# Performance work log

Hardware: AMD Instinct MI355X
Metric: run time of the kernel (lower is better)

## Reference

```python
import jax, jax.numpy as jnp
import numpy as np

D_MODEL, D_FF, N_EXPERTS, P = 512, 2048, 16, 128
B, S = 8, 512


def setup_inputs() -> dict:
    key = jax.random.key(0)
    ks = jax.random.split(key, 16)
    T = B * S
    g = lambda k, shape, fan: (jax.random.normal(k, shape, jnp.float32) * (fan ** -0.5))
    return {
        "x": jax.random.normal(ks[0], (B, S, D_MODEL), jnp.float32),
        "h_prev": jax.random.normal(ks[1], (T, P), jnp.float32),
        # projector: Linear(d_model -> p)
        "Wp": g(ks[2], (P, D_MODEL), D_MODEL), "bp": jnp.zeros((P,), jnp.float32),
        # GRUCell(p, p): torch layout [3p, p] in (r, z, n) order
        "W_ih": g(ks[3], (3 * P, P), P), "W_hh": g(ks[4], (3 * P, P), P),
        "b_ih": jnp.zeros((3 * P,), jnp.float32), "b_hh": jnp.zeros((3 * P,), jnp.float32),
        # router: Linear(p -> num_experts)
        "Wr": g(ks[5], (N_EXPERTS, P), P), "br": jnp.zeros((N_EXPERTS,), jnp.float32),
        # experts: Linear(d, dff) -> ReLU -> Linear(dff, d), stacked over experts
        "W1": g(ks[6], (N_EXPERTS, D_MODEL, D_FF), D_MODEL),
        "b1": jnp.zeros((N_EXPERTS, D_FF), jnp.float32),
        "W2": g(ks[7], (N_EXPERTS, D_FF, D_MODEL), D_FF),
        "b2": jnp.zeros((N_EXPERTS, D_MODEL), jnp.float32),
        "k": 2,
    }


def reference(x, h_prev, Wp, bp, W_ih, W_hh, b_ih, b_hh, Wr, br, W1, b1, W2, b2, k):
    Bsz, Seq, d = x.shape
    xf = x.reshape(-1, d)                      # [T, d]
    xp = xf @ Wp.T + bp                        # [T, p]
    # GRUCell (torch semantics, gate order r,z,n)
    gx = xp @ W_ih.T + b_ih                    # [T, 3p]
    gh = h_prev @ W_hh.T + b_hh                # [T, 3p]
    xr, xz, xn = jnp.split(gx, 3, axis=-1)
    hr, hz, hn = jnp.split(gh, 3, axis=-1)
    r = jax.nn.sigmoid(xr + hr)
    z = jax.nn.sigmoid(xz + hz)
    n = jnp.tanh(xn + r * hn)
    h = (1.0 - z) * n + z * h_prev             # [T, p]
    # router -> top-k, renormalized
    probs = jax.nn.softmax(h @ Wr.T + br, axis=-1)       # [T, E]
    top_p, top_i = jax.lax.top_k(probs, k)               # [T, k]
    top_p = top_p / jnp.sum(top_p, axis=-1, keepdims=True)
    T = xf.shape[0]
    E = Wr.shape[0]
    # dense combine weights: cw[t, e] = renorm prob if e in top-k else 0
    cw = jnp.zeros((T, E), x.dtype).at[jnp.arange(T)[:, None], top_i].set(top_p)
    out = jnp.zeros_like(xf)
    for e in range(E):  # fixed small expert count; per-expert GEMM, masked combine
        y = jax.nn.relu(xf @ W1[e] + b1[e]) @ W2[e] + b2[e]
        out = out + cw[:, e:e + 1] * y
    return out.reshape(Bsz, Seq, d), h
```

## Files before the change

kernel.cpp:

```cpp
#include <hip/hip_runtime.h>
#include <cmath>

#define T_TOK 4096
#define DM    512
#define DFF   2048
#define NE    16
#define PP    128
#define WROW  520

typedef __attribute__((ext_vector_type(8))) short bfrag;
typedef __attribute__((ext_vector_type(4))) float f32x4;
typedef __attribute__((ext_vector_type(8))) unsigned short us8;

__device__ __forceinline__ unsigned short f2bf(float f) {
  unsigned int u = __float_as_uint(f);
  unsigned int r = (u + 0x7FFFu + ((u >> 16) & 1u)) >> 16;
  return (unsigned short)r;
}
__device__ __forceinline__ float bf2f(unsigned short b) {
  return __uint_as_float(((unsigned int)b) << 16);
}

__global__ __launch_bounds__(256) void sgemm_nt_bias(
    const float* __restrict__ A, const float* __restrict__ B,
    const float* __restrict__ bias, float* __restrict__ C,
    int M, int N, int K)
{
  __shared__ __align__(16) float As[16][68];
  __shared__ __align__(16) float Bs[16][68];
  const int bm = blockIdx.x * 64;
  const int bn = blockIdx.y * 64;
  const int tid = threadIdx.x;
  const int tx = tid & 15;
  const int ty = tid >> 4;

  float acc[4][4] = {{0.f}};

  for (int k0 = 0; k0 < K; k0 += 16) {
    {
      int r  = tid >> 2;
      int c4 = (tid & 3) * 4;
      float4 v = *(const float4*)(A + (size_t)(bm + r) * K + k0 + c4);
      As[c4+0][r] = v.x; As[c4+1][r] = v.y; As[c4+2][r] = v.z; As[c4+3][r] = v.w;
    }
    {
      int r  = tid >> 2;
      int c4 = (tid & 3) * 4;
      float4 v = *(const float4*)(B + (size_t)(bn + r) * K + k0 + c4);
      Bs[c4+0][r] = v.x; Bs[c4+1][r] = v.y; Bs[c4+2][r] = v.z; Bs[c4+3][r] = v.w;
    }
    __syncthreads();
    #pragma unroll
    for (int k = 0; k < 16; ++k) {
      float4 a4 = *(const float4*)&As[k][ty*4];
      float4 b4 = *(const float4*)&Bs[k][tx*4];
      float a[4] = {a4.x, a4.y, a4.z, a4.w};
      float b[4] = {b4.x, b4.y, b4.z, b4.w};
      #pragma unroll
      for (int i = 0; i < 4; ++i)
        #pragma unroll
        for (int j = 0; j < 4; ++j)
          acc[i][j] += a[i] * b[j];
    }
    __syncthreads();
  }
  #pragma unroll
  for (int i = 0; i < 4; ++i) {
    int row = bm + ty*4 + i;
    #pragma unroll
    for (int j = 0; j < 4; ++j) {
      int col = bn + tx*4 + j;
      C[(size_t)row * N + col] = acc[i][j] + bias[col];
    }
  }
}

__global__ __launch_bounds__(256) void sgemm_cat(
    const float* __restrict__ A1, const float* __restrict__ A2,
    const float* __restrict__ B, const float* __restrict__ bias,
    float* __restrict__ C)
{
  __shared__ __align__(16) float As[16][68];
  __shared__ __align__(16) float Bs[16][68];
  const int bm = blockIdx.x * 64;
  const int bn = blockIdx.y * 64;
  const int tid = threadIdx.x;
  const int tx = tid & 15;
  const int ty = tid >> 4;

  float acc[4][4] = {{0.f}};

  for (int k0 = 0; k0 < 256; k0 += 16) {
    {
      int r  = tid >> 2;
      int c4 = (tid & 3) * 4;
      const float* src = (k0 < 128) ? (A1 + (size_t)(bm + r) * 128 + k0 + c4)
                                    : (A2 + (size_t)(bm + r) * 128 + (k0 - 128) + c4);
      float4 v = *(const float4*)src;
      As[c4+0][r] = v.x; As[c4+1][r] = v.y; As[c4+2][r] = v.z; As[c4+3][r] = v.w;
    }
    {
      int r  = tid >> 2;
      int c4 = (tid & 3) * 4;
      float4 v = *(const float4*)(B + (size_t)(bn + r) * 256 + k0 + c4);
      Bs[c4+0][r] = v.x; Bs[c4+1][r] = v.y; Bs[c4+2][r] = v.z; Bs[c4+3][r] = v.w;
    }
    __syncthreads();
    #pragma unroll
    for (int k = 0; k < 16; ++k) {
      float4 a4 = *(const float4*)&As[k][ty*4];
      float4 b4 = *(const float4*)&Bs[k][tx*4];
      float a[4] = {a4.x, a4.y, a4.z, a4.w};
      float b[4] = {b4.x, b4.y, b4.z, b4.w};
      #pragma unroll
      for (int i = 0; i < 4; ++i)
        #pragma unroll
        for (int j = 0; j < 4; ++j)
          acc[i][j] += a[i] * b[j];
    }
    __syncthreads();
  }
  #pragma unroll
  for (int i = 0; i < 4; ++i) {
    int row = bm + ty*4 + i;
    #pragma unroll
    for (int j = 0; j < 4; ++j) {
      int col = bn + tx*4 + j;
      C[(size_t)row * 512 + col] = acc[i][j] + bias[col];
    }
  }
}

__global__ void prep_gates(const float* __restrict__ W_ih, const float* __restrict__ W_hh,
                           const float* __restrict__ b_ih, const float* __restrict__ b_hh,
                           float* __restrict__ Bcat, float* __restrict__ bcat,
                           int* __restrict__ cnt)
{
  int id = blockIdx.x * 256 + threadIdx.x;
  if (blockIdx.x == 0 && threadIdx.x < NE) cnt[threadIdx.x] = 0;
  int n = id >> 8, k = id & 255;
  float v;
  if (n < 256)      v = (k < 128) ? W_ih[n * 128 + k] : W_hh[n * 128 + k - 128];
  else if (n < 384) v = (k < 128) ? W_ih[n * 128 + k] : 0.f;
  else              v = (k < 128) ? 0.f : W_hh[(n - 128) * 128 + k - 128];
  Bcat[n * 256 + k] = v;
  if (id < 512) {
    float b = (id < 256) ? (b_ih[id] + b_hh[id])
            : (id < 384) ? b_ih[id] : b_hh[id - 128];
    bcat[id] = b;
  }
}

__global__ void gru_elem2(const float* __restrict__ s, const float* __restrict__ hprev,
                          float* __restrict__ hout)
{
  int i = blockIdx.x * blockDim.x + threadIdx.x;
  int t = i >> 7, p = i & 127;
  const float* sr = s + (size_t)t * 512;
  float rz = sr[p], zz = sr[128 + p], xn = sr[256 + p], hn = sr[384 + p];
  float r = 1.f / (1.f + expf(-rz));
  float z = 1.f / (1.f + expf(-zz));
  float n = tanhf(xn + r * hn);
  hout[i] = (1.f - z) * n + z * hprev[i];
}

__global__ __launch_bounds__(64) void router_topk2(
    const float* __restrict__ h, const float* __restrict__ Wr,
    const float* __restrict__ br,
    float* __restrict__ wgt, int* __restrict__ tokslot,
    int* __restrict__ cnt)
{
  __shared__ float4 wr4[NE * 32];
  __shared__ float br_s[NE];
  __shared__ int hist[NE];
  __shared__ int basex[NE];

  int tid = threadIdx.x;
  #pragma unroll
  for (int i = 0; i < 8; ++i)
    wr4[tid + i * 64] = ((const float4*)Wr)[tid + i * 64];
  if (tid < NE) { br_s[tid] = br[tid]; hist[tid] = 0; }
  __syncthreads();

  int t = blockIdx.x * 64 + tid;
  const float4* hr = (const float4*)(h + (size_t)t * PP);

  float logit[NE];
  #pragma unroll
  for (int e = 0; e < NE; ++e) logit[e] = 0.f;
  #pragma unroll 4
  for (int i = 0; i < 32; ++i) {
    float4 v = hr[i];
    #pragma unroll
    for (int e = 0; e < NE; ++e) {
      float4 w = wr4[e * 32 + i];
      logit[e] += v.x * w.x + v.y * w.y + v.z * w.z + v.w * w.w;
    }
  }
  #pragma unroll
  for (int e = 0; e < NE; ++e) logit[e] += br_s[e];

  float mx = logit[0];
  #pragma unroll
  for (int e = 1; e < NE; ++e) mx = fmaxf(mx, logit[e]);
  float p[NE];
  #pragma unroll
  for (int e = 0; e < NE; ++e) p[e] = expf(logit[e] - mx);
  int i0 = 0; float m0 = p[0];
  #pragma unroll
  for (int e = 1; e < NE; ++e) { if (p[e] > m0) { m0 = p[e]; i0 = e; } }
  int i1 = -1; float m1 = -1.f;
  #pragma unroll
  for (int e = 0; e < NE; ++e) { if (e != i0 && p[e] > m1) { m1 = p[e]; i1 = e; } }
  float inv = 1.f / (m0 + m1);
  float w0 = m0 * inv, w1 = m1 * inv;

  int r0 = atomicAdd(&hist[i0], 1);
  int r1 = atomicAdd(&hist[i1], 1);
  __syncthreads();
  if (tid < NE && hist[tid] > 0) basex[tid] = atomicAdd(&cnt[tid], hist[tid]);
  __syncthreads();

  int p0 = basex[i0] + r0;
  tokslot[(size_t)i0 * T_TOK + p0] = (t << 1);
  wgt[(size_t)i0 * T_TOK + p0] = w0;
  int p1 = basex[i1] + r1;
  tokslot[(size_t)i1 * T_TOK + p1] = (t << 1) | 1;
  wgt[(size_t)i1 * T_TOK + p1] = w1;
}

__global__ void calc_off(const int* __restrict__ cnt, int* __restrict__ offPad) {
  if (threadIdx.x == 0) {
    int s = 0;
    for (int e = 0; e < NE; ++e) { offPad[e] = s; s += (cnt[e] + 127) & ~127; }
    offPad[NE] = s;
  }
}

__global__ __launch_bounds__(256) void gather_x(
    const float* __restrict__ x, const int* __restrict__ tokslot,
    const int* __restrict__ cnt, const int* __restrict__ offPad,
    unsigned short* __restrict__ xg)
{
  int e = blockIdx.y;
  int n = cnt[e];
  int npad = (n + 127) & ~127;
  int r0 = blockIdx.x * 128;
  if (r0 >= npad) return;
  int t = threadIdx.x;
  int r = r0 + (t >> 1);
  int half = t & 1;
  unsigned short* orow = xg + (size_t)(offPad[e] + r) * DM + half * 256;
  if (r >= n) {
    us8 z = {0,0,0,0,0,0,0,0};
    #pragma unroll
    for (int i = 0; i < 32; ++i) *(us8*)(orow + i * 8) = z;
    return;
  }
  int tok = tokslot[(size_t)e * T_TOK + r] >> 1;
  const float* irow = x + (size_t)tok * DM + half * 256;
  #pragma unroll
  for (int i = 0; i < 32; ++i) {
    float4 a = *(const float4*)(irow + i * 8);
    float4 b = *(const float4*)(irow + i * 8 + 4);
    us8 o;
    o[0]=f2bf(a.x); o[1]=f2bf(a.y); o[2]=f2bf(a.z); o[3]=f2bf(a.w);
    o[4]=f2bf(b.x); o[5]=f2bf(b.y); o[6]=f2bf(b.z); o[7]=f2bf(b.w);
    *(us8*)(orow + i * 8) = o;
  }
}

__global__ __launch_bounds__(512, 2) void expert_gemm1(
    const unsigned short* __restrict__ xg, const float* __restrict__ W1,
    const float* __restrict__ b1,
    const int* __restrict__ cnt, const int* __restrict__ offPad,
    unsigned short* __restrict__ hidden)
{
  __shared__ unsigned short wlds[64 * WROW];
  int bid = blockIdx.x;
  int xcd = bid & 7, j = bid >> 3;
  int e  = xcd * 2 + (j >> 5);
  int nb = (j & 31) * 64;
  int t = threadIdx.x, lane = t & 63, wv = t >> 6;
  int l15 = lane & 15, lg = lane >> 4;
  int wm = wv * 32;

  {
    const float* w1src = W1 + (size_t)e * DM * DFF + nb;
    int c4 = (t & 15) * 4, rr = t >> 4;
    #pragma unroll
    for (int pass = 0; pass < 16; ++pass) {
      int r = rr + pass * 32;
      float4 v = *(const float4*)(w1src + (size_t)r * DFF + c4);
      wlds[(c4+0) * WROW + r] = f2bf(v.x);
      wlds[(c4+1) * WROW + r] = f2bf(v.y);
      wlds[(c4+2) * WROW + r] = f2bf(v.z);
      wlds[(c4+3) * WROW + r] = f2bf(v.w);
    }
  }
  __syncthreads();

  int npad = (cnt[e] + 127) & ~127;
  int ebase = offPad[e];

  for (int tb = 0; tb < npad; tb += 256) {
    int r0 = wm, r1 = wm + 16;
    if (tb + r0 >= npad) r0 -= 128;
    if (tb + r1 >= npad) r1 -= 128;
    const unsigned short* a0p = xg + (size_t)(ebase + tb + r0 + l15) * DM;
    const unsigned short* a1p = xg + (size_t)(ebase + tb + r1 + l15) * DM;

    f32x4 acc[2][4];
    #pragma unroll
    for (int i = 0; i < 2; ++i)
      #pragma unroll
      for (int jj = 0; jj < 4; ++jj) acc[i][jj] = (f32x4){0.f, 0.f, 0.f, 0.f};

    #pragma unroll 2
    for (int kt = 0; kt < 8; ++kt) {
      #pragma unroll
      for (int kk = 0; kk < 2; ++kk) {
        int cidx = kt * 8 + kk * 4 + lg;
        bfrag a0 = *(const bfrag*)(a0p + (cidx << 3));
        bfrag a1 = *(const bfrag*)(a1p + (cidx << 3));
        bfrag b0 = *(const bfrag*)&wlds[(0 * 16 + l15) * WROW + cidx * 8];
        bfrag b1f = *(const bfrag*)&wlds[(1 * 16 + l15) * WROW + cidx * 8];
        bfrag b2 = *(const bfrag*)&wlds[(2 * 16 + l15) * WROW + cidx * 8];
        bfrag b3 = *(const bfrag*)&wlds[(3 * 16 + l15) * WROW + cidx * 8];
        acc[0][0] = __builtin_amdgcn_mfma_f32_16x16x32_bf16(a0, b0,  acc[0][0], 0, 0, 0);
        acc[0][1] = __builtin_amdgcn_mfma_f32_16x16x32_bf16(a0, b1f, acc[0][1], 0, 0, 0);
        acc[0][2] = __builtin_amdgcn_mfma_f32_16x16x32_bf16(a0, b2,  acc[0][2], 0, 0, 0);
        acc[0][3] = __builtin_amdgcn_mfma_f32_16x16x32_bf16(a0, b3,  acc[0][3], 0, 0, 0);
        acc[1][0] = __builtin_amdgcn_mfma_f32_16x16x32_bf16(a1, b0,  acc[1][0], 0, 0, 0);
        acc[1][1] = __builtin_amdgcn_mfma_f32_16x16x32_bf16(a1, b1f, acc[1][1], 0, 0, 0);
        acc[1][2] = __builtin_amdgcn_mfma_f32_16x16x32_bf16(a1, b2,  acc[1][2], 0, 0, 0);
        acc[1][3] = __builtin_amdgcn_mfma_f32_16x16x32_bf16(a1, b3,  acc[1][3], 0, 0, 0);
      }
    }

    int roff0 = r0, roff1 = r1;
    #pragma unroll
    for (int fj = 0; fj < 4; ++fj) {
      int col = nb + fj * 16 + l15;
      float bias = b1[(size_t)e * DFF + col];
      #pragma unroll
      for (int rg = 0; rg < 4; ++rg) {
        int rowA = ebase + tb + roff0 + lg * 4 + rg;
        float vA = acc[0][fj][rg] + bias;
        hidden[(size_t)rowA * DFF + col] = f2bf(vA > 0.f ? vA : 0.f);
        int rowB = ebase + tb + roff1 + lg * 4 + rg;
        float vB = acc[1][fj][rg] + bias;
        hidden[(size_t)rowB * DFF + col] = f2bf(vB > 0.f ? vB : 0.f);
      }
    }
  }
}

__global__ __launch_bounds__(512, 4) void expert_gemm2(
    const unsigned short* __restrict__ hidden, const float* __restrict__ W2,
    const float* __restrict__ b2,
    const int* __restrict__ cnt, const int* __restrict__ offPad,
    const int* __restrict__ tokslot, const float* __restrict__ wgt,
    unsigned short* __restrict__ planes)
{
  __shared__ unsigned short wlds[64 * WROW];
  int bid = blockIdx.x;
  int xcd = bid & 7, j = bid >> 3;
  int e   = xcd * 2 + (j >> 5);
  int r5  = j & 31;
  int ncb = (r5 & 7) * 64;
  int kq  = r5 >> 3;
  int kb  = kq * 512;
  int t = threadIdx.x, lane = t & 63, wv = t >> 6;
  int l15 = lane & 15, lg = lane >> 4;
  int wm = wv * 32;

  {
    const float* w2src = W2 + (size_t)e * DFF * DM + (size_t)kb * DM + ncb;
    int c4 = (t & 15) * 4, fr = t >> 4;
    #pragma unroll
    for (int pass = 0; pass < 16; ++pass) {
      int f = fr + pass * 32;
      float4 v = *(const float4*)(w2src + (size_t)f * DM + c4);
      wlds[(c4+0) * WROW + f] = f2bf(v.x);
      wlds[(c4+1) * WROW + f] = f2bf(v.y);
      wlds[(c4+2) * WROW + f] = f2bf(v.z);
      wlds[(c4+3) * WROW + f] = f2bf(v.w);
    }
  }
  __syncthreads();

  int n = cnt[e];
  int npad = (n + 127) & ~127;
  int ebase = offPad[e];

  for (int tb = 0; tb < npad; tb += 256) {
    int roff[2];
    #pragma unroll
    for (int fi = 0; fi < 2; ++fi) {
      int r0 = wm + fi * 16;
      roff[fi] = (tb + r0 >= npad) ? r0 - 128 : r0;
    }
    f32x4 acc[2][4];
    #pragma unroll
    for (int i = 0; i < 2; ++i)
      #pragma unroll
      for (int jj = 0; jj < 4; ++jj) acc[i][jj] = (f32x4){0.f, 0.f, 0.f, 0.f};

    #pragma unroll 2
    for (int kt = 0; kt < 8; ++kt) {
      #pragma unroll
      for (int kk = 0; kk < 2; ++kk) {
        int cidx = kt * 8 + kk * 4 + lg;
        bfrag a[2], b[4];
        #pragma unroll
        for (int fi = 0; fi < 2; ++fi)
          a[fi] = *(const bfrag*)(hidden + (size_t)(ebase + tb + roff[fi] + l15) * DFF + kb + (cidx << 3));
        #pragma unroll
        for (int fj = 0; fj < 4; ++fj) {
          int row = fj * 16 + l15;
          b[fj] = *(const bfrag*)&wlds[row * WROW + cidx * 8];
        }
        #pragma unroll
        for (int fi = 0; fi < 2; ++fi)
          #pragma unroll
          for (int fj = 0; fj < 4; ++fj)
            acc[fi][fj] = __builtin_amdgcn_mfma_f32_16x16x32_bf16(a[fi], b[fj], acc[fi][fj], 0, 0, 0);
      }
    }

    #pragma unroll
    for (int fi = 0; fi < 2; ++fi) {
      #pragma unroll
      for (int rg = 0; rg < 4; ++rg) {
        int idx = tb + roff[fi] + lg * 4 + rg;
        if (idx >= n) continue;
        int ts = tokslot[(size_t)e * T_TOK + idx];
        float w = wgt[(size_t)e * T_TOK + idx];
        unsigned short* pl = planes + ((size_t)(kq * 2 + (ts & 1)) * T_TOK + (ts >> 1)) * DM;
        #pragma unroll
        for (int fj = 0; fj < 4; ++fj) {
          int col = ncb + fj * 16 + l15;
          float bv = (kq == 0) ? b2[(size_t)e * DM + col] : 0.f;
          pl[col] = f2bf((acc[fi][fj][rg] + bv) * w);
        }
      }
    }
  }
}

__global__ __launch_bounds__(256) void combine_out(
    const unsigned short* __restrict__ planes, float* __restrict__ out)
{
  int i = blockIdx.x * blockDim.x + threadIdx.x;
  float s[8] = {0.f};
  #pragma unroll
  for (int pl = 0; pl < 8; ++pl) {
    us8 v = *(const us8*)&planes[(size_t)pl * T_TOK * DM + (size_t)i * 8];
    #pragma unroll
    for (int jj = 0; jj < 8; ++jj) s[jj] += bf2f(v[jj]);
  }
  float4* o = (float4*)(out + (size_t)i * 8);
  o[0] = make_float4(s[0], s[1], s[2], s[3]);
  o[1] = make_float4(s[4], s[5], s[6], s[7]);
}

extern "C" void kernel_launch(void* const* d_in, const int* in_sizes, int n_in,
                              void* d_out, int out_size, void* d_ws, size_t ws_size,
                              hipStream_t stream)
{
  const float* x      = (const float*)d_in[0];
  const float* h_prev = (const float*)d_in[1];
  const float* Wp     = (const float*)d_in[2];
  const float* bp     = (const float*)d_in[3];
  const float* W_ih   = (const float*)d_in[4];
  const float* W_hh   = (const float*)d_in[5];
  const float* b_ih   = (const float*)d_in[6];
  const float* b_hh   = (const float*)d_in[7];
  const float* Wr     = (const float*)d_in[8];
  const float* br     = (const float*)d_in[9];
  const float* W1     = (const float*)d_in[10];
  const float* b1     = (const float*)d_in[11];
  const float* W2     = (const float*)d_in[12];
  const float* b2     = (const float*)d_in[13];
  (void)in_sizes; (void)n_in; (void)out_size; (void)ws_size;

  float* out  = (float*)d_out;
  float* hout = out + (size_t)T_TOK * DM;

  char* ws = (char*)d_ws;
  unsigned short* planes = (unsigned short*)(ws + 0);
  unsigned short* hidden = (unsigned short*)(ws + 35651584);
  unsigned short* xg     = (unsigned short*)(ws + 79691776);
  float* xp   = (float*)(ws + 92274688);
  float* gs   = (float*)(ws + 94371840);
  float* Bcat = (float*)(ws + 102760448);
  float* bcat = (float*)(ws + 103284736);
  float* wgt  = (float*)(ws + 103809024);
  int* tokslot = (int*)(ws + 104071168);
  int* cnt     = (int*)(ws + 104333312);
  int* offPad  = (int*)(ws + 104333376);

  prep_gates<<<512, 256, 0, stream>>>(W_ih, W_hh, b_ih, b_hh, Bcat, bcat, cnt);
  sgemm_nt_bias<<<dim3(T_TOK/64, PP/64), 256, 0, stream>>>(x, Wp, bp, xp, T_TOK, PP, DM);
  sgemm_cat<<<dim3(T_TOK/64, 512/64), 256, 0, stream>>>(xp, h_prev, Bcat, bcat, gs);
  gru_elem2<<<(T_TOK * PP) / 256, 256, 0, stream>>>(gs, h_prev, hout);
  router_topk2<<<64, 64, 0, stream>>>(hout, Wr, br, wgt, tokslot, cnt);
  calc_off<<<1, 64, 0, stream>>>(cnt, offPad);

  gather_x<<<dim3(32, NE), 256, 0, stream>>>(x, tokslot, cnt, offPad, xg);
  expert_gemm1<<<512, 512, 0, stream>>>(xg, W1, b1, cnt, offPad, hidden);
  expert_gemm2<<<512, 512, 0, stream>>>(hidden, W2, b2, cnt, offPad, tokslot, wgt, planes);
  combine_out<<<(T_TOK * DM / 8) / 256, 256, 0, stream>>>(planes, out);
}
```

Measured before the change: 242.7 us.

## Pre-transpose W2 to bf16 in fused prep kernel and async-load into LDS

Adds a fused prep kernel that merges the x·Wp projection, the GRU gate-matrix packing and a new pass that transposes W2 into a bf16 [E, DM, DFF] buffer. expert_gemm2 then fills its LDS tile with direct global_load_lds 16-byte copies into an XOR-swizzled layout, instead of converting fp32 to bf16 and doing scattered transposed LDS stores per block. The intent is to remove the slow strided transpose-convert from the expert GEMM's prologue and cut one kernel launch. In exchange, the full W2 (16M elements) is read and rewritten every call, and the workspace layout is reorganised.

```diff
diff --git a/kernel.cpp b/kernel.cpp
--- a/kernel.cpp
+++ b/kernel.cpp
@@ -21,56 +21,99 @@
   return __uint_as_float(((unsigned int)b) << 16);
 }
 
-__global__ __launch_bounds__(256) void sgemm_nt_bias(
-    const float* __restrict__ A, const float* __restrict__ B,
-    const float* __restrict__ bias, float* __restrict__ C,
-    int M, int N, int K)
-{
-  __shared__ __align__(16) float As[16][68];
-  __shared__ __align__(16) float Bs[16][68];
-  const int bm = blockIdx.x * 64;
-  const int bn = blockIdx.y * 64;
+#define GLOAD_LDS16(g, l) __builtin_amdgcn_global_load_lds( \
+    (const __attribute__((address_space(1))) void*)(g), \
+    (__attribute__((address_space(3))) void*)(l), 16, 0, 0)
+
+__global__ __launch_bounds__(256) void prep_fused(
+    const float* __restrict__ x, const float* __restrict__ Wp,
+    const float* __restrict__ bp, float* __restrict__ xp,
+    const float* __restrict__ W2, unsigned short* __restrict__ W2t,
+    const float* __restrict__ W_ih, const float* __restrict__ W_hh,
+    const float* __restrict__ b_ih, const float* __restrict__ b_hh,
+    float* __restrict__ Bcat, float* __restrict__ bcat, int* __restrict__ cnt)
+{
+  __shared__ __align__(16) char smem[16640];
+  const int bid = blockIdx.x;
   const int tid = threadIdx.x;
-  const int tx = tid & 15;
-  const int ty = tid >> 4;
-
-  float acc[4][4] = {{0.f}};
-
-  for (int k0 = 0; k0 < K; k0 += 16) {
-    {
-      int r  = tid >> 2;
-      int c4 = (tid & 3) * 4;
-      float4 v = *(const float4*)(A + (size_t)(bm + r) * K + k0 + c4);
-      As[c4+0][r] = v.x; As[c4+1][r] = v.y; As[c4+2][r] = v.z; As[c4+3][r] = v.w;
-    }
-    {
-      int r  = tid >> 2;
-      int c4 = (tid & 3) * 4;
-      float4 v = *(const float4*)(B + (size_t)(bn + r) * K + k0 + c4);
-      Bs[c4+0][r] = v.x; Bs[c4+1][r] = v.y; Bs[c4+2][r] = v.z; Bs[c4+3][r] = v.w;
+
+  if (bid < 128) {
+    float (*As)[68] = (float (*)[68])smem;
+    float (*Bs)[68] = (float (*)[68])(smem + 4352);
+    const int bm = (bid >> 1) * 64;
+    const int bn = (bid & 1) * 64;
+    const int tx = tid & 15, ty = tid >> 4;
+    float acc[4][4] = {{0.f}};
+    for (int k0 = 0; k0 < DM; k0 += 16) {
+      {
+        int r = tid >> 2, c4 = (tid & 3) * 4;
+        float4 v = *(const float4*)(x + (size_t)(bm + r) * DM + k0 + c4);
+        As[c4+0][r] = v.x; As[c4+1][r] = v.y; As[c4+2][r] = v.z; As[c4+3][r] = v.w;
+      }
+      {
+        int r = tid >> 2, c4 = (tid & 3) * 4;
+        float4 v = *(const float4*)(Wp + (size_t)(bn + r) * DM + k0 + c4);
+        Bs[c4+0][r] = v.x; Bs[c4+1][r] = v.y; Bs[c4+2][r] = v.z; Bs[c4+3][r] = v.w;
+      }
+      __syncthreads();
+      #pragma unroll
+      for (int k = 0; k < 16; ++k) {
+        float4 a4 = *(const float4*)&As[k][ty*4];
+        float4 b4 = *(const float4*)&Bs[k][tx*4];
+        float a[4] = {a4.x, a4.y, a4.z, a4.w};
+        float b[4] = {b4.x, b4.y, b4.z, b4.w};
+        #pragma unroll
+        for (int i = 0; i < 4; ++i)
+          #pragma unroll
+          for (int j = 0; j < 4; ++j)
+            acc[i][j] += a[i] * b[j];
+      }
+      __syncthreads();
+    }
+    #pragma unroll
+    for (int i = 0; i < 4; ++i)
+      #pragma unroll
+      for (int j = 0; j < 4; ++j)
+        xp[(size_t)(bm + ty*4 + i) * PP + bn + tx*4 + j] = acc[i][j] + bp[bn + tx*4 + j];
+
+  } else if (bid < 4224) {
+    float (*tl)[65] = (float (*)[65])smem;
+    int u = bid - 128;
+    int nt = u & 7, kt = (u >> 3) & 31, e = u >> 8;
+    const float* ib = W2 + (size_t)e * DFF * DM + (size_t)(kt * 64) * DM + nt * 64;
+    int r = tid >> 2, c0 = (tid & 3) * 16;
+    #pragma unroll
+    for (int i = 0; i < 4; ++i) {
+      float4 v = *(const float4*)(ib + (size_t)r * DM + c0 + i * 4);
+      tl[r][c0+i*4+0] = v.x; tl[r][c0+i*4+1] = v.y;
+      tl[r][c0+i*4+2] = v.z; tl[r][c0+i*4+3] = v.w;
     }
     __syncthreads();
-    #pragma unroll
-    for (int k = 0; k < 16; ++k) {
-      float4 a4 = *(const float4*)&As[k][ty*4];
-      float4 b4 = *(const float4*)&Bs[k][tx*4];
-      float a[4] = {a4.x, a4.y, a4.z, a4.w};
-      float b[4] = {b4.x, b4.y, b4.z, b4.w};
-      #pragma unroll
-      for (int i = 0; i < 4; ++i)
-        #pragma unroll
-        for (int j = 0; j < 4; ++j)
-          acc[i][j] += a[i] * b[j];
-    }
-    __syncthreads();
-  }
-  #pragma unroll
-  for (int i = 0; i < 4; ++i) {
-    int row = bm + ty*4 + i;
-    #pragma unroll
-    for (int j = 0; j < 4; ++j) {
-      int col = bn + tx*4 + j;
-      C[(size_t)row * N + col] = acc[i][j] + bias[col];
+    unsigned short* ob = W2t + (size_t)e * DM * DFF + (size_t)(nt * 64) * DFF + kt * 64;
+    #pragma unroll
+    for (int i = 0; i < 2; ++i) {
+      int uu = tid + i * 256;
+      int n = uu >> 3, k0 = (uu & 7) * 8;
+      us8 o;
+      #pragma unroll
+      for (int j = 0; j < 8; ++j) o[j] = f2bf(tl[k0 + j][n]);
+      *(us8*)(ob + (size_t)n * DFF + k0) = o;
+    }
+
+  } else {
+    int blk = bid - 4224;
+    int id = blk * 256 + tid;
+    if (blk == 0 && tid < NE) cnt[tid] = 0;
+    int n = id >> 8, k = id & 255;
+    float v;
+    if (n < 256)      v = (k < 128) ? W_ih[n * 128 + k] : W_hh[n * 128 + k - 128];
+    else if (n < 384) v = (k < 128) ? W_ih[n * 128 + k] : 0.f;
+    else              v = (k < 128) ? 0.f : W_hh[(n - 128) * 128 + k - 128];
+    Bcat[n * 256 + k] = v;
+    if (id < 512) {
+      float b = (id < 256) ? (b_ih[id] + b_hh[id])
+              : (id < 384) ? b_ih[id] : b_hh[id - 128];
+      bcat[id] = b;
     }
   }
 }
@@ -128,26 +171,6 @@
       int col = bn + tx*4 + j;
       C[(size_t)row * 512 + col] = acc[i][j] + bias[col];
     }
-  }
-}
-
-__global__ void prep_gates(const float* __restrict__ W_ih, const float* __restrict__ W_hh,
-                           const float* __restrict__ b_ih, const float* __restrict__ b_hh,
-                           float* __restrict__ Bcat, float* __restrict__ bcat,
-                           int* __restrict__ cnt)
-{
-  int id = blockIdx.x * 256 + threadIdx.x;
-  if (blockIdx.x == 0 && threadIdx.x < NE) cnt[threadIdx.x] = 0;
-  int n = id >> 8, k = id & 255;
-  float v;
-  if (n < 256)      v = (k < 128) ? W_ih[n * 128 + k] : W_hh[n * 128 + k - 128];
-  else if (n < 384) v = (k < 128) ? W_ih[n * 128 + k] : 0.f;
-  else              v = (k < 128) ? 0.f : W_hh[(n - 128) * 128 + k - 128];
-  Bcat[n * 256 + k] = v;
-  if (id < 512) {
-    float b = (id < 256) ? (b_ih[id] + b_hh[id])
-            : (id < 384) ? b_ih[id] : b_hh[id - 128];
-    bcat[id] = b;
   }
 }
 
@@ -357,13 +380,13 @@
 }
 
 __global__ __launch_bounds__(512, 4) void expert_gemm2(
-    const unsigned short* __restrict__ hidden, const float* __restrict__ W2,
+    const unsigned short* __restrict__ hidden, const unsigned short* __restrict__ W2t,
     const float* __restrict__ b2,
     const int* __restrict__ cnt, const int* __restrict__ offPad,
     const int* __restrict__ tokslot, const float* __restrict__ wgt,
     unsigned short* __restrict__ planes)
 {
-  __shared__ unsigned short wlds[64 * WROW];
+  __shared__ unsigned short wlds[64 * 512];
   int bid = blockIdx.x;
   int xcd = bid & 7, j = bid >> 3;
   int e   = xcd * 2 + (j >> 5);
@@ -375,18 +398,13 @@
   int l15 = lane & 15, lg = lane >> 4;
   int wm = wv * 32;
 
-  {
-    const float* w2src = W2 + (size_t)e * DFF * DM + (size_t)kb * DM + ncb;
-    int c4 = (t & 15) * 4, fr = t >> 4;
-    #pragma unroll
-    for (int pass = 0; pass < 16; ++pass) {
-      int f = fr + pass * 32;
-      float4 v = *(const float4*)(w2src + (size_t)f * DM + c4);
-      wlds[(c4+0) * WROW + f] = f2bf(v.x);
-      wlds[(c4+1) * WROW + f] = f2bf(v.y);
-      wlds[(c4+2) * WROW + f] = f2bf(v.z);
-      wlds[(c4+3) * WROW + f] = f2bf(v.w);
-    }
+  const unsigned short* w2b = W2t + ((size_t)e * DM + ncb) * DFF + kb;
+  #pragma unroll
+  for (int i = 0; i < 8; ++i) {
+    int s = t + i * 512;
+    int r = s >> 6, c = s & 63;
+    int cs = (c & 56) | ((c & 7) ^ (r & 7));
+    GLOAD_LDS16(w2b + (size_t)r * DFF + (cs << 3), &wlds[s * 8]);
   }
   __syncthreads();
 
@@ -419,7 +437,8 @@
         #pragma unroll
         for (int fj = 0; fj < 4; ++fj) {
           int row = fj * 16 + l15;
-          b[fj] = *(const bfrag*)&wlds[row * WROW + cidx * 8];
+          int cs = (cidx & 56) | ((cidx & 7) ^ (row & 7));
+          b[fj] = *(const bfrag*)&wlds[row * 512 + (cs << 3)];
         }
         #pragma unroll
         for (int fi = 0; fi < 2; ++fi)
@@ -490,19 +509,20 @@
 
   char* ws = (char*)d_ws;
   unsigned short* planes = (unsigned short*)(ws + 0);
-  unsigned short* hidden = (unsigned short*)(ws + 35651584);
-  unsigned short* xg     = (unsigned short*)(ws + 79691776);
-  float* xp   = (float*)(ws + 92274688);
-  float* gs   = (float*)(ws + 94371840);
-  float* Bcat = (float*)(ws + 102760448);
-  float* bcat = (float*)(ws + 103284736);
-  float* wgt  = (float*)(ws + 103809024);
-  int* tokslot = (int*)(ws + 104071168);
-  int* cnt     = (int*)(ws + 104333312);
-  int* offPad  = (int*)(ws + 104333376);
-
-  prep_gates<<<512, 256, 0, stream>>>(W_ih, W_hh, b_ih, b_hh, Bcat, bcat, cnt);
-  sgemm_nt_bias<<<dim3(T_TOK/64, PP/64), 256, 0, stream>>>(x, Wp, bp, xp, T_TOK, PP, DM);
+  float* xp   = (float*)(ws + 0);
+  float* gs   = (float*)(ws + 2097152);
+  float* Bcat = (float*)(ws + 10485760);
+  float* bcat = (float*)(ws + 11010048);
+  unsigned short* W2t = (unsigned short*)(ws + 33554432);
+  unsigned short* hidden = (unsigned short*)(ws + 67108864);
+  unsigned short* xg = (unsigned short*)(ws + 109051904);
+  float* wgt   = (float*)(ws + 119537664);
+  int* tokslot = (int*)(ws + 119799808);
+  int* cnt     = (int*)(ws + 120061952);
+  int* offPad  = (int*)(ws + 120062016);
+
+  prep_fused<<<4736, 256, 0, stream>>>(x, Wp, bp, xp, W2, W2t,
+                                       W_ih, W_hh, b_ih, b_hh, Bcat, bcat, cnt);
   sgemm_cat<<<dim3(T_TOK/64, 512/64), 256, 0, stream>>>(xp, h_prev, Bcat, bcat, gs);
   gru_elem2<<<(T_TOK * PP) / 256, 256, 0, stream>>>(gs, h_prev, hout);
   router_topk2<<<64, 64, 0, stream>>>(hout, Wr, br, wgt, tokslot, cnt);
@@ -510,6 +530,6 @@
 
   gather_x<<<dim3(32, NE), 256, 0, stream>>>(x, tokslot, cnt, offPad, xg);
   expert_gemm1<<<512, 512, 0, stream>>>(xg, W1, b1, cnt, offPad, hidden);
-  expert_gemm2<<<512, 512, 0, stream>>>(hidden, W2, b2, cnt, offPad, tokslot, wgt, planes);
+  expert_gemm2<<<512, 512, 0, stream>>>(hidden, W2t, b2, cnt, offPad, tokslot, wgt, planes);
   combine_out<<<(T_TOK * DM / 8) / 256, 256, 0, stream>>>(planes, out);
 }
```

Measured after the change: 244.9 us (median of 2 runs). No clear change (+0.9%).
